# Kernel optimization log

Hardware: AMD Instinct MI355X
Metric: run time of the kernel (lower is better)

The kernel has to match this reference:

```python
import jax, jax.numpy as jnp
import numpy as np

LN_EPS = 1e-5

def setup_inputs() -> dict:
    key = jax.random.key(0)
    ks = jax.random.split(key, 12)
    B, S, D = 4, 2048, 1024
    s = 1.0 / np.sqrt(D)
    return {
        "query": jax.random.normal(ks[0], (B, S, D), jnp.float32),
        "key_in": jax.random.normal(ks[1], (B, S, D), jnp.float32),
        "value": jax.random.normal(ks[2], (B, S, D), jnp.float32),
        "Wq": jax.random.normal(ks[3], (D, D), jnp.float32) * s,
        "bq": jax.random.normal(ks[4], (D,), jnp.float32) * s,
        "Wk": jax.random.normal(ks[5], (D, D), jnp.float32) * s,
        "bk": jax.random.normal(ks[6], (D,), jnp.float32) * s,
        "Wv": jax.random.normal(ks[7], (D, D), jnp.float32) * s,
        "bv": jax.random.normal(ks[8], (D,), jnp.float32) * s,
        "gamma": jnp.ones((D,), jnp.float32),
        "beta": jnp.zeros((D,), jnp.float32),
    }

def reference(query, key_in, value, Wq, bq, Wk, bk, Wv, bv, gamma, beta):
    # Linear projections (torch Linear: x @ W^T + b; here W stored as [in,out])
    q = jnp.einsum('bsd,df->bsf', query, Wq) + bq
    k = jnp.einsum('bsd,df->bsf', key_in, Wk) + bk
    v = jnp.einsum('bsd,df->bsf', value, Wv) + bv
    # Attention: note NO 1/sqrt(d) scaling, single head (faithful to source)
    attn = jnp.einsum('bqd,bkd->bqk', q, k)          # [B,S,S]
    probs = jax.nn.softmax(attn, axis=-1)
    result = jnp.einsum('bqk,bkd->bqd', probs, v)     # [B,S,D]
    # Residual + LayerNorm
    x = result + query
    mu = jnp.mean(x, axis=-1, keepdims=True)
    var = jnp.mean((x - mu) ** 2, axis=-1, keepdims=True)
    return (x - mu) * jax.lax.rsqrt(var + LN_EPS) * gamma + beta
```

## Files before the change

### kernel.cpp

```cpp
#include <hip/hip_runtime.h>
#include <hip/hip_bf16.h>
#include <cstdint>


typedef unsigned short u16;
typedef unsigned int   u32;
typedef _Float16 f16;
typedef f16   f16x8  __attribute__((ext_vector_type(8)));
typedef f16   f16x4  __attribute__((ext_vector_type(4)));
typedef float f32x4  __attribute__((ext_vector_type(4)));

#define DEV __device__ __forceinline__

DEV void gld_lds16(const f16* g, char* l){
  __builtin_amdgcn_global_load_lds(
      (const __attribute__((address_space(1))) u32*)(uintptr_t)g,
      (__attribute__((address_space(3))) u32*)(u32)(uintptr_t)l, 16, 0, 0);
}

DEV int swz_lid(){
  int lid = (blockIdx.z * gridDim.y + blockIdx.y) * gridDim.x + blockIdx.x;
  int cpx = (gridDim.x * gridDim.y * gridDim.z) >> 3;
  return (lid & 7) * cpx + (lid >> 3);
}

#define MFMA_(av, bv, ci, cj) \
  acc[ci][cj] = __builtin_amdgcn_mfma_f32_16x16x32_f16(av, bv, acc[ci][cj], 0, 0, 0)

template<bool MORE>
DEV void ktile_body(const f16* (&src)[8], char* bufc, char* stash,
                    int ob0, int ob1, int rA, int rB, int sk0, int sk1,
                    f32x4 (&acc)[8][4])
{
  f16x8 a0[4], a1[4], b0[2], b1[2], b2[2], b3[2];

  if (MORE){ gld_lds16(src[0], stash + 0 + ob0); src[0] += 64;
             gld_lds16(src[1], stash + 0 + ob1); src[1] += 64; }
  if (MORE) asm volatile("s_waitcnt vmcnt(6)\ns_barrier" ::: "memory");
  else      asm volatile("s_waitcnt vmcnt(4)\ns_barrier" ::: "memory");
#pragma unroll
  for (int i = 0; i < 4; i++) a0[i] = *(const f16x8*)(bufc + (i << 12) + rA + sk0);
  b0[0] = *(const f16x8*)(bufc + 32768 +    0 + rB + sk0);
  b0[1] = *(const f16x8*)(bufc + 32768 + 8192 + rB + sk0);
  __builtin_amdgcn_s_setprio(1);
#pragma unroll
  for (int i = 0; i < 4; i++){ MFMA_(a0[i], b0[0], i, 0); MFMA_(a0[i], b0[1], i, 1); }
  __builtin_amdgcn_s_setprio(0);

  if (MORE){ gld_lds16(src[2], stash + 32768 + ob0); src[2] += 64;
             gld_lds16(src[3], stash + 32768 + ob1); src[3] += 64; }
#pragma unroll
  for (int i = 0; i < 4; i++) a1[i] = *(const f16x8*)(bufc + (i << 12) + rA + sk1);
  b1[0] = *(const f16x8*)(bufc + 32768 +    0 + rB + sk1);
  b1[1] = *(const f16x8*)(bufc + 32768 + 8192 + rB + sk1);
  __builtin_amdgcn_s_setprio(1);
#pragma unroll
  for (int i = 0; i < 4; i++){ MFMA_(a1[i], b1[0], i, 0); MFMA_(a1[i], b1[1], i, 1); }
  __builtin_amdgcn_s_setprio(0);

  if (MORE){ gld_lds16(src[4], stash + 16384 + ob0); src[4] += 64;
             gld_lds16(src[5], stash + 16384 + ob1); src[5] += 64; }
  if (MORE) asm volatile("s_waitcnt vmcnt(6)\ns_barrier" ::: "memory");
  else      asm volatile("s_waitcnt vmcnt(0)\ns_barrier" ::: "memory");
  b2[0] = *(const f16x8*)(bufc + 49152 +    0 + rB + sk0);
  b2[1] = *(const f16x8*)(bufc + 49152 + 8192 + rB + sk0);
  __builtin_amdgcn_s_setprio(1);
#pragma unroll
  for (int i = 0; i < 4; i++){ MFMA_(a0[i], b2[0], i, 2); MFMA_(a0[i], b2[1], i, 3); }
  __builtin_amdgcn_s_setprio(0);

  if (MORE){ gld_lds16(src[6], stash + 49152 + ob0); src[6] += 64;
             gld_lds16(src[7], stash + 49152 + ob1); src[7] += 64; }
  b3[0] = *(const f16x8*)(bufc + 49152 +    0 + rB + sk1);
  b3[1] = *(const f16x8*)(bufc + 49152 + 8192 + rB + sk1);
  __builtin_amdgcn_s_setprio(1);
#pragma unroll
  for (int i = 0; i < 4; i++){ MFMA_(a1[i], b3[0], i, 2); MFMA_(a1[i], b3[1], i, 3); }
  __builtin_amdgcn_s_setprio(0);

#pragma unroll
  for (int i = 0; i < 4; i++) a0[i] = *(const f16x8*)(bufc + 16384 + (i << 12) + rA + sk0);
  __builtin_amdgcn_s_setprio(1);
#pragma unroll
  for (int i = 0; i < 4; i++){ MFMA_(a0[i], b0[0], 4 + i, 0); MFMA_(a0[i], b0[1], 4 + i, 1); }
  __builtin_amdgcn_s_setprio(0);

#pragma unroll
  for (int i = 0; i < 4; i++) a1[i] = *(const f16x8*)(bufc + 16384 + (i << 12) + rA + sk1);
  __builtin_amdgcn_s_setprio(1);
#pragma unroll
  for (int i = 0; i < 4; i++){ MFMA_(a1[i], b1[0], 4 + i, 0); MFMA_(a1[i], b1[1], 4 + i, 1); }
  __builtin_amdgcn_s_setprio(0);

  __builtin_amdgcn_s_setprio(1);
#pragma unroll
  for (int i = 0; i < 4; i++){ MFMA_(a0[i], b2[0], 4 + i, 2); MFMA_(a0[i], b2[1], 4 + i, 3); }
  __builtin_amdgcn_s_setprio(0);

  __builtin_amdgcn_s_setprio(1);
#pragma unroll
  for (int i = 0; i < 4; i++){ MFMA_(a1[i], b3[0], 4 + i, 2); MFMA_(a1[i], b3[1], 4 + i, 3); }
  __builtin_amdgcn_s_setprio(0);
}

DEV void gemm_core(const f16* __restrict__ A, int lda,
                   const f16* __restrict__ B, int ldb,
                   int nt, char* smem, f32x4 (&acc)[8][4])
{
  const int tid  = threadIdx.x;
  const int lane = tid & 63;
  const int wv   = tid >> 6;
  const int wm   = wv >> 2, wn = wv & 3;
  const int lr   = lane & 15, lq = lane >> 4;

  const int ob0 = tid * 16;
  const int ob1 = ob0 + 8192;
  const int r0  = ob0 >> 7, r1 = ob1 >> 7;
  const int sl0 = ((ob0 >> 4) & 7) ^ (r0 & 7);
  const int sl1 = ((ob1 >> 4) & 7) ^ (r1 & 7);
  const f16* src[8];
  src[0] = A + (size_t)r0 * lda + sl0 * 8;
  src[1] = A + (size_t)r1 * lda + sl1 * 8;
  src[2] = B + (size_t)r0 * ldb + sl0 * 8;
  src[3] = B + (size_t)r1 * ldb + sl1 * 8;
  src[4] = A + (size_t)(128 + r0) * lda + sl0 * 8;
  src[5] = A + (size_t)(128 + r1) * lda + sl1 * 8;
  src[6] = B + (size_t)(128 + r0) * ldb + sl0 * 8;
  src[7] = B + (size_t)(128 + r1) * ldb + sl1 * 8;

  const int rA  = (wm * 16 + lr) << 7;
  const int rB  = (wn * 16 + lr) << 7;
  const int sk0 = ((lq ^ (lane & 7)) << 4);
  const int sk1 = (((4 | lq) ^ (lane & 7)) << 4);

#pragma unroll
  for (int i = 0; i < 8; i++)
#pragma unroll
    for (int j = 0; j < 4; j++) acc[i][j] = (f32x4){0.f, 0.f, 0.f, 0.f};

  gld_lds16(src[0], smem +     0 + ob0); src[0] += 64;
  gld_lds16(src[1], smem +     0 + ob1); src[1] += 64;
  gld_lds16(src[2], smem + 32768 + ob0); src[2] += 64;
  gld_lds16(src[3], smem + 32768 + ob1); src[3] += 64;
  gld_lds16(src[4], smem + 16384 + ob0); src[4] += 64;
  gld_lds16(src[5], smem + 16384 + ob1); src[5] += 64;
  gld_lds16(src[6], smem + 49152 + ob0); src[6] += 64;
  gld_lds16(src[7], smem + 49152 + ob1); src[7] += 64;

  for (int t = 0; t < nt - 1; ++t){
    char* bufc  = smem + ((t & 1) << 16);
    char* stash = smem + (((t & 1) ^ 1) << 16);
    ktile_body<true>(src, bufc, stash, ob0, ob1, rA, rB, sk0, sk1, acc);
  }
  {
    char* bufc  = smem + (((nt - 1) & 1) << 16);
    char* stash = smem + ((((nt - 1) & 1) ^ 1) << 16);
    ktile_body<false>(src, bufc, stash, ob0, ob1, rA, rB, sk0, sk1, acc);
  }
}

__global__ __launch_bounds__(512, 2) void proj8p(
    const f16* __restrict__ xq, const f16* __restrict__ xk, const f16* __restrict__ xv,
    const f16* __restrict__ wq, const f16* __restrict__ wk, const f16* __restrict__ wv,
    const float* __restrict__ bq, const float* __restrict__ bk, const float* __restrict__ bv,
    f16* __restrict__ oq, f16* __restrict__ ok, f16* __restrict__ ovT)
{
  __shared__ char smem[131072];
  const int s  = swz_lid();
  const int bx = s & 3, by = (s >> 2) & 31, z = s >> 7;
  const int m0 = by * 256, n0 = bx * 256;
  const f16* A = (z == 0 ? xq : z == 1 ? xk : xv) + (size_t)m0 * 1024;
  const f16* B = (z == 0 ? wq : z == 1 ? wk : wv) + (size_t)n0 * 1024;
  const float* bias = (z == 0 ? bq : z == 1 ? bk : bv);

  f32x4 acc[8][4];
  gemm_core(A, 1024, B, 1024, 16, smem, acc);

  const int lane = threadIdx.x & 63;
  const int wv_  = threadIdx.x >> 6;
  const int wm = wv_ >> 2, wn = wv_ & 3;
  const int lr = lane & 15, rj = (lane >> 4) * 4;

  if (z < 2){
    f16* o = z ? ok : oq;
#pragma unroll
    for (int i = 0; i < 8; i++)
#pragma unroll
      for (int j = 0; j < 4; j++){
        int row = m0 + i * 32 + wm * 16 + rj;
        int col = n0 + j * 64 + wn * 16 + lr;
        float bvl = bias[col];
#pragma unroll
        for (int r = 0; r < 4; r++)
          o[(size_t)(row + r) * 1024 + col] = (f16)(acc[i][j][r] + bvl);
      }
  } else {
#pragma unroll
    for (int i = 0; i < 8; i++)
#pragma unroll
      for (int j = 0; j < 4; j++){
        int row = m0 + i * 32 + wm * 16 + rj;
        int col = n0 + j * 64 + wn * 16 + lr;
        float bvl = bias[col];
        f16x4 tv;
#pragma unroll
        for (int r = 0; r < 4; r++) tv[r] = (f16)(acc[i][j][r] + bvl);
        *(f16x4*)(ovT + (size_t)col * 8192 + row) = tv;
      }
  }
}

__global__ __launch_bounds__(512, 2) void qk8p(
    const f16* __restrict__ q, const f16* __restrict__ k, float* __restrict__ Sout)
{
  __shared__ char smem[131072];
  const int s  = swz_lid();
  const int bx = s & 7, by = (s >> 3) & 7, z = s >> 6;
  const int m0 = by * 256, n0 = bx * 256;
  const f16* A = q + (size_t)z * 2048 * 1024 + (size_t)m0 * 1024;
  const f16* B = k + (size_t)z * 2048 * 1024 + (size_t)n0 * 1024;

  f32x4 acc[8][4];
  gemm_core(A, 1024, B, 1024, 16, smem, acc);

  const int lane = threadIdx.x & 63;
  const int wv_  = threadIdx.x >> 6;
  const int wm = wv_ >> 2, wn = wv_ & 3;
  const int lr = lane & 15, rj = (lane >> 4) * 4;
  float* o = Sout + (size_t)z * 2048 * 2048;
#pragma unroll
  for (int i = 0; i < 8; i++)
#pragma unroll
    for (int j = 0; j < 4; j++){
      int row = m0 + i * 32 + wm * 16 + rj;
      int col = n0 + j * 64 + wn * 16 + lr;
#pragma unroll
      for (int r = 0; r < 4; r++)
        o[(size_t)(row + r) * 2048 + col] = acc[i][j][r];
    }
}

__global__ __launch_bounds__(512, 2) void pv8p(
    const f16* __restrict__ P, const f16* __restrict__ vT, float* __restrict__ O)
{
  __shared__ char smem[131072];
  const int s  = swz_lid();
  const int bx = s & 3, by = (s >> 2) & 7, z = s >> 5;
  const int zb = z >> 1, h = z & 1;
  const int m0 = by * 256, n0 = bx * 256;
  const f16* A = P  + (size_t)zb * 2048 * 2048 + (size_t)m0 * 2048 + h * 1024;
  const f16* B = vT + (size_t)n0 * 8192 + (size_t)zb * 2048 + h * 1024;

  f32x4 acc[8][4];
  gemm_core(A, 2048, B, 8192, 16, smem, acc);

  const int lane = threadIdx.x & 63;
  const int wv_  = threadIdx.x >> 6;
  const int wm = wv_ >> 2, wn = wv_ & 3;
  const int lr = lane & 15, rj = (lane >> 4) * 4;
  float* o = O + (size_t)h * 8388608 + (size_t)zb * 2048 * 1024;
#pragma unroll
  for (int i = 0; i < 8; i++)
#pragma unroll
    for (int j = 0; j < 4; j++){
      int row = m0 + i * 32 + wm * 16 + rj;
      int col = n0 + j * 64 + wn * 16 + lr;
#pragma unroll
      for (int r = 0; r < 4; r++)
        o[(size_t)(row + r) * 1024 + col] = acc[i][j][r];
    }
}

__global__ __launch_bounds__(256) void cvt3_f32_f16(
    const float* __restrict__ x0, const float* __restrict__ x1, const float* __restrict__ x2,
    f16* __restrict__ y0, f16* __restrict__ y1, f16* __restrict__ y2){
  const int z = blockIdx.y;
  const float* x = z == 0 ? x0 : z == 1 ? x1 : x2;
  f16* y = z == 0 ? y0 : z == 1 ? y1 : y2;
  int i = (blockIdx.x * 256 + threadIdx.x) * 8;
  float4 a = *(const float4*)(x + i);
  float4 b = *(const float4*)(x + i + 4);
  f16x8 v;
  v[0]=(f16)a.x; v[1]=(f16)a.y; v[2]=(f16)a.z; v[3]=(f16)a.w;
  v[4]=(f16)b.x; v[5]=(f16)b.y; v[6]=(f16)b.z; v[7]=(f16)b.w;
  *(f16x8*)(y + i) = v;
}

__global__ __launch_bounds__(256) void transpose3_cvt_w(
    const float* __restrict__ W0, const float* __restrict__ W1, const float* __restrict__ W2,
    f16* __restrict__ T0, f16* __restrict__ T1, f16* __restrict__ T2, int D){
  const int z = blockIdx.z;
  const float* W = z == 0 ? W0 : z == 1 ? W1 : W2;
  f16* T = z == 0 ? T0 : z == 1 ? T1 : T2;
  __shared__ float t[32][33];
  int tx = threadIdx.x & 31, ty = threadIdx.x >> 5;
  int bx = blockIdx.x * 32, by = blockIdx.y * 32;
#pragma unroll
  for (int j = 0; j < 4; j++) t[ty + j*8][tx] = W[(size_t)(by + ty + j*8) * D + bx + tx];
  __syncthreads();
#pragma unroll
  for (int j = 0; j < 4; j++){
    float v = t[tx][ty + j*8];
    T[(size_t)(bx + ty + j*8) * D + by + tx] = (f16)v;
  }
}

DEV float wred_max(float v){
#pragma unroll
  for (int o = 32; o; o >>= 1) v = fmaxf(v, __shfl_xor(v, o));
  return v;
}
DEV float wred_sum(float v){
#pragma unroll
  for (int o = 32; o; o >>= 1) v += __shfl_xor(v, o);
  return v;
}

__global__ __launch_bounds__(256) void softmax_rows(const float* __restrict__ S, f16* __restrict__ P){
  const int row = blockIdx.x;
  const int tid = threadIdx.x;
  const float* x = S + (size_t)row * 2048 + tid * 8;
  f16* p = P + (size_t)row * 2048 + tid * 8;
  float4 a = *(const float4*)x, b = *(const float4*)(x + 4);
  float v[8] = {a.x, a.y, a.z, a.w, b.x, b.y, b.z, b.w};
  __shared__ float red[4];

  float m = v[0];
#pragma unroll
  for (int j = 1; j < 8; j++) m = fmaxf(m, v[j]);
  m = wred_max(m);
  if ((tid & 63) == 0) red[tid >> 6] = m;
  __syncthreads();
  m = fmaxf(fmaxf(red[0], red[1]), fmaxf(red[2], red[3]));

  float s = 0.f;
#pragma unroll
  for (int j = 0; j < 8; j++){ v[j] = __expf(v[j] - m); s += v[j]; }
  s = wred_sum(s);
  __syncthreads();
  if ((tid & 63) == 0) red[tid >> 6] = s;
  __syncthreads();
  s = red[0] + red[1] + red[2] + red[3];

  float inv = 1.f / s;
  f16x8 o;
#pragma unroll
  for (int j = 0; j < 8; j++) o[j] = (f16)(v[j] * inv);
  *(f16x8*)p = o;
}

__global__ __launch_bounds__(256) void resid_ln2(const float* __restrict__ O0,
                                                 const float* __restrict__ O1,
                                                 const float* __restrict__ query,
                                                 const float* __restrict__ gamma,
                                                 const float* __restrict__ beta,
                                                 float* __restrict__ out){
  const int row = blockIdx.x;
  const int tid = threadIdx.x;
  const size_t base = (size_t)row * 1024 + tid * 4;
  float4 o4 = *(const float4*)(O0 + base);
  float4 p4 = *(const float4*)(O1 + base);
  float4 q4 = *(const float4*)(query + base);
  float x[4] = {o4.x + p4.x + q4.x, o4.y + p4.y + q4.y,
                o4.z + p4.z + q4.z, o4.w + p4.w + q4.w};
  float s = 0.f, ss = 0.f;
#pragma unroll
  for (int j = 0; j < 4; j++){ s += x[j]; ss += x[j] * x[j]; }

  __shared__ float red[4];
  s = wred_sum(s);
  if ((tid & 63) == 0) red[tid >> 6] = s;
  __syncthreads();
  s = red[0] + red[1] + red[2] + red[3];
  ss = wred_sum(ss);
  __syncthreads();
  if ((tid & 63) == 0) red[tid >> 6] = ss;
  __syncthreads();
  ss = red[0] + red[1] + red[2] + red[3];

  float mu = s * (1.f / 1024.f);
  float var = ss * (1.f / 1024.f) - mu * mu;
  float rs = rsqrtf(var + 1e-5f);
  float4 g4 = *(const float4*)(gamma + tid * 4);
  float4 b4 = *(const float4*)(beta + tid * 4);
  float4 r;
  r.x = (x[0] - mu) * rs * g4.x + b4.x;
  r.y = (x[1] - mu) * rs * g4.y + b4.y;
  r.z = (x[2] - mu) * rs * g4.z + b4.z;
  r.w = (x[3] - mu) * rs * g4.w + b4.w;
  *(float4*)(out + base) = r;
}

extern "C" void kernel_launch(void* const* d_in, const int* in_sizes, int n_in,
                              void* d_out, int out_size, void* d_ws, size_t ws_size,
                              hipStream_t stream){
  const float* query  = (const float*)d_in[0];
  const float* key_in = (const float*)d_in[1];
  const float* value  = (const float*)d_in[2];
  const float* Wq = (const float*)d_in[3];
  const float* bq = (const float*)d_in[4];
  const float* Wk = (const float*)d_in[5];
  const float* bk = (const float*)d_in[6];
  const float* Wv = (const float*)d_in[7];
  const float* bv = (const float*)d_in[8];
  const float* gamma = (const float*)d_in[9];
  const float* beta  = (const float*)d_in[10];

  const int B = 4, S = 2048, D = 1024;
  const int M = B * S;
  const size_t MB = 1ull << 20;
  char* ws = (char*)d_ws;

  f16* qf16 = (f16*)(ws + 0);
  f16* kf16 = (f16*)(ws + 16 * MB);
  f16* vT   = (f16*)(ws + 32 * MB);
  f16* wt_q = (f16*)(ws + 48 * MB);
  f16* wt_k = (f16*)(ws + 50 * MB);
  f16* wt_v = (f16*)(ws + 52 * MB);
  float* Obuf = (float*)(ws + 54 * MB);
  f16* xq   = (f16*)(ws + 118 * MB);
  f16* xk   = (f16*)(ws + 134 * MB);
  f16* xv   = (f16*)(ws + 150 * MB);
  float* Sbuf = (float*)(ws + 118 * MB);
  f16*   Pbuf = (f16*)(ws + 182 * MB);

  dim3 blk(256);
  const int nElem = M * D;

  cvt3_f32_f16<<<dim3(nElem / 2048, 3), blk, 0, stream>>>(query, key_in, value, xq, xk, xv);
  transpose3_cvt_w<<<dim3(32, 32, 3), blk, 0, stream>>>(Wq, Wk, Wv, wt_q, wt_k, wt_v, D);

  proj8p<<<dim3(4, 32, 3), dim3(512), 0, stream>>>(xq, xk, xv, wt_q, wt_k, wt_v,
                                                   bq, bk, bv, qf16, kf16, vT);

  qk8p<<<dim3(8, 8, 4), dim3(512), 0, stream>>>(qf16, kf16, Sbuf);

  softmax_rows<<<M, blk, 0, stream>>>(Sbuf, Pbuf);

  pv8p<<<dim3(4, 8, 8), dim3(512), 0, stream>>>(Pbuf, vT, Obuf);

  resid_ln2<<<M, blk, 0, stream>>>(Obuf, Obuf + 8388608, query, gamma, beta, (float*)d_out);
}
```

Before: 199.0 us.

## Restructure GEMM k-tile into four phases with batched LDS reads and barriers

Reorganizes the k-tile body of the shared GEMM core into four phases. Each phase issues all its LDS fragment reads for both k-halves up front, then the next global-to-LDS prefetch, then a barrier with lgkmcnt wait fenced by sched_barrier, then a dense MFMA cluster. The prefetch issue order changes so the B second half loads before the A second half, with adjusted vmcnt thresholds and an extra prologue wait. The goal is fewer interleaved LDS waits and more back-to-back MFMA issue, at the cost of extra barriers per tile and more live fragment registers.

```diff
diff --git a/kernel.cpp b/kernel.cpp
--- a/kernel.cpp
+++ b/kernel.cpp
@@ -27,80 +27,87 @@
 #define MFMA_(av, bv, ci, cj) \
   acc[ci][cj] = __builtin_amdgcn_mfma_f32_16x16x32_f16(av, bv, acc[ci][cj], 0, 0, 0)
 
+#define PHASE_SYNC() do { \
+  __builtin_amdgcn_sched_barrier(0); \
+  __builtin_amdgcn_s_barrier(); \
+  asm volatile("s_waitcnt lgkmcnt(0)" ::: "memory"); \
+  __builtin_amdgcn_sched_barrier(0); } while(0)
+
 template<bool MORE>
 DEV void ktile_body(const f16* (&src)[8], char* bufc, char* stash,
                     int ob0, int ob1, int rA, int rB, int sk0, int sk1,
                     f32x4 (&acc)[8][4])
 {
-  f16x8 a0[4], a1[4], b0[2], b1[2], b2[2], b3[2];
-
-  if (MORE){ gld_lds16(src[0], stash + 0 + ob0); src[0] += 64;
-             gld_lds16(src[1], stash + 0 + ob1); src[1] += 64; }
-  if (MORE) asm volatile("s_waitcnt vmcnt(6)\ns_barrier" ::: "memory");
-  else      asm volatile("s_waitcnt vmcnt(4)\ns_barrier" ::: "memory");
-#pragma unroll
-  for (int i = 0; i < 4; i++) a0[i] = *(const f16x8*)(bufc + (i << 12) + rA + sk0);
-  b0[0] = *(const f16x8*)(bufc + 32768 +    0 + rB + sk0);
-  b0[1] = *(const f16x8*)(bufc + 32768 + 8192 + rB + sk0);
+  f16x8 a[4][2], b[4][2];
+
+#pragma unroll
+  for (int i = 0; i < 4; i++){
+    a[i][0] = *(const f16x8*)(bufc + (i << 12) + rA + sk0);
+    a[i][1] = *(const f16x8*)(bufc + (i << 12) + rA + sk1);
+  }
+#pragma unroll
+  for (int j = 0; j < 2; j++){
+    b[j][0] = *(const f16x8*)(bufc + 32768 + (j << 13) + rB + sk0);
+    b[j][1] = *(const f16x8*)(bufc + 32768 + (j << 13) + rB + sk1);
+  }
+  if (MORE){ gld_lds16(src[0], stash + ob0); src[0] += 64;
+             gld_lds16(src[1], stash + ob1); src[1] += 64; }
+  PHASE_SYNC();
   __builtin_amdgcn_s_setprio(1);
 #pragma unroll
-  for (int i = 0; i < 4; i++){ MFMA_(a0[i], b0[0], i, 0); MFMA_(a0[i], b0[1], i, 1); }
+  for (int i = 0; i < 4; i++)
+#pragma unroll
+    for (int j = 0; j < 2; j++){ MFMA_(a[i][0], b[j][0], i, j); MFMA_(a[i][1], b[j][1], i, j); }
   __builtin_amdgcn_s_setprio(0);
-
+  __builtin_amdgcn_sched_barrier(0);
+  if (MORE) asm volatile("s_waitcnt vmcnt(4)\ns_barrier" ::: "memory");
+  else      asm volatile("s_waitcnt vmcnt(2)\ns_barrier" ::: "memory");
+
+#pragma unroll
+  for (int j = 0; j < 2; j++){
+    b[2 + j][0] = *(const f16x8*)(bufc + 49152 + (j << 13) + rB + sk0);
+    b[2 + j][1] = *(const f16x8*)(bufc + 49152 + (j << 13) + rB + sk1);
+  }
   if (MORE){ gld_lds16(src[2], stash + 32768 + ob0); src[2] += 64;
              gld_lds16(src[3], stash + 32768 + ob1); src[3] += 64; }
-#pragma unroll
-  for (int i = 0; i < 4; i++) a1[i] = *(const f16x8*)(bufc + (i << 12) + rA + sk1);
-  b1[0] = *(const f16x8*)(bufc + 32768 +    0 + rB + sk1);
-  b1[1] = *(const f16x8*)(bufc + 32768 + 8192 + rB + sk1);
+  PHASE_SYNC();
   __builtin_amdgcn_s_setprio(1);
 #pragma unroll
-  for (int i = 0; i < 4; i++){ MFMA_(a1[i], b1[0], i, 0); MFMA_(a1[i], b1[1], i, 1); }
+  for (int i = 0; i < 4; i++)
+#pragma unroll
+    for (int j = 2; j < 4; j++){ MFMA_(a[i][0], b[j][0], i, j); MFMA_(a[i][1], b[j][1], i, j); }
   __builtin_amdgcn_s_setprio(0);
+  __builtin_amdgcn_sched_barrier(0);
+  if (MORE) asm volatile("s_waitcnt vmcnt(4)\ns_barrier" ::: "memory");
+  else      asm volatile("s_waitcnt vmcnt(0)\ns_barrier" ::: "memory");
+
+#pragma unroll
+  for (int i = 0; i < 4; i++){
+    a[i][0] = *(const f16x8*)(bufc + 16384 + (i << 12) + rA + sk0);
+    a[i][1] = *(const f16x8*)(bufc + 16384 + (i << 12) + rA + sk1);
+  }
+  if (MORE){ gld_lds16(src[6], stash + 49152 + ob0); src[6] += 64;
+             gld_lds16(src[7], stash + 49152 + ob1); src[7] += 64; }
+  PHASE_SYNC();
+  __builtin_amdgcn_s_setprio(1);
+#pragma unroll
+  for (int i = 0; i < 4; i++)
+#pragma unroll
+    for (int j = 0; j < 2; j++){ MFMA_(a[i][0], b[j][0], 4 + i, j); MFMA_(a[i][1], b[j][1], 4 + i, j); }
+  __builtin_amdgcn_s_setprio(0);
+  __builtin_amdgcn_sched_barrier(0);
+  asm volatile("s_barrier" ::: "memory");
 
   if (MORE){ gld_lds16(src[4], stash + 16384 + ob0); src[4] += 64;
              gld_lds16(src[5], stash + 16384 + ob1); src[5] += 64; }
-  if (MORE) asm volatile("s_waitcnt vmcnt(6)\ns_barrier" ::: "memory");
-  else      asm volatile("s_waitcnt vmcnt(0)\ns_barrier" ::: "memory");
-  b2[0] = *(const f16x8*)(bufc + 49152 +    0 + rB + sk0);
-  b2[1] = *(const f16x8*)(bufc + 49152 + 8192 + rB + sk0);
   __builtin_amdgcn_s_setprio(1);
 #pragma unroll
-  for (int i = 0; i < 4; i++){ MFMA_(a0[i], b2[0], i, 2); MFMA_(a0[i], b2[1], i, 3); }
+  for (int i = 0; i < 4; i++)
+#pragma unroll
+    for (int j = 2; j < 4; j++){ MFMA_(a[i][0], b[j][0], 4 + i, j); MFMA_(a[i][1], b[j][1], 4 + i, j); }
   __builtin_amdgcn_s_setprio(0);
-
-  if (MORE){ gld_lds16(src[6], stash + 49152 + ob0); src[6] += 64;
-             gld_lds16(src[7], stash + 49152 + ob1); src[7] += 64; }
-  b3[0] = *(const f16x8*)(bufc + 49152 +    0 + rB + sk1);
-  b3[1] = *(const f16x8*)(bufc + 49152 + 8192 + rB + sk1);
-  __builtin_amdgcn_s_setprio(1);
-#pragma unroll
-  for (int i = 0; i < 4; i++){ MFMA_(a1[i], b3[0], i, 2); MFMA_(a1[i], b3[1], i, 3); }
-  __builtin_amdgcn_s_setprio(0);
-
-#pragma unroll
-  for (int i = 0; i < 4; i++) a0[i] = *(const f16x8*)(bufc + 16384 + (i << 12) + rA + sk0);
-  __builtin_amdgcn_s_setprio(1);
-#pragma unroll
-  for (int i = 0; i < 4; i++){ MFMA_(a0[i], b0[0], 4 + i, 0); MFMA_(a0[i], b0[1], 4 + i, 1); }
-  __builtin_amdgcn_s_setprio(0);
-
-#pragma unroll
-  for (int i = 0; i < 4; i++) a1[i] = *(const f16x8*)(bufc + 16384 + (i << 12) + rA + sk1);
-  __builtin_amdgcn_s_setprio(1);
-#pragma unroll
-  for (int i = 0; i < 4; i++){ MFMA_(a1[i], b1[0], 4 + i, 0); MFMA_(a1[i], b1[1], 4 + i, 1); }
-  __builtin_amdgcn_s_setprio(0);
-
-  __builtin_amdgcn_s_setprio(1);
-#pragma unroll
-  for (int i = 0; i < 4; i++){ MFMA_(a0[i], b2[0], 4 + i, 2); MFMA_(a0[i], b2[1], 4 + i, 3); }
-  __builtin_amdgcn_s_setprio(0);
-
-  __builtin_amdgcn_s_setprio(1);
-#pragma unroll
-  for (int i = 0; i < 4; i++){ MFMA_(a1[i], b3[0], 4 + i, 2); MFMA_(a1[i], b3[1], 4 + i, 3); }
-  __builtin_amdgcn_s_setprio(0);
+  __builtin_amdgcn_sched_barrier(0);
+  if (MORE) asm volatile("s_waitcnt vmcnt(4)\ns_barrier" ::: "memory");
 }
 
 DEV void gemm_core(const f16* __restrict__ A, int lda,
@@ -142,10 +149,11 @@
   gld_lds16(src[1], smem +     0 + ob1); src[1] += 64;
   gld_lds16(src[2], smem + 32768 + ob0); src[2] += 64;
   gld_lds16(src[3], smem + 32768 + ob1); src[3] += 64;
+  gld_lds16(src[6], smem + 49152 + ob0); src[6] += 64;
+  gld_lds16(src[7], smem + 49152 + ob1); src[7] += 64;
   gld_lds16(src[4], smem + 16384 + ob0); src[4] += 64;
   gld_lds16(src[5], smem + 16384 + ob1); src[5] += 64;
-  gld_lds16(src[6], smem + 49152 + ob0); src[6] += 64;
-  gld_lds16(src[7], smem + 49152 + ob1); src[7] += 64;
+  asm volatile("s_waitcnt vmcnt(4)\ns_barrier" ::: "memory");
 
   for (int t = 0; t < nt - 1; ++t){
     char* bufc  = smem + ((t & 1) << 16);
```

New measurement: 210.0 us. 1.06x slower.
